# Kernel tuning notes

Hardware: AMD Instinct MI355X
Metric: run time of the kernel (lower is better)

Reference implementation:

```python
import jax, jax.numpy as jnp
import numpy as np

CLASS_NUM = 4            # number of positive classes
NUM_CLASSES = CLASS_NUM + 1  # last column is the negative class
W_P = 4.0
EPS = 1e-9
THR = 0.5


def setup_inputs() -> dict:
    key = jax.random.key(0)
    k1, k2 = jax.random.split(key)
    N = 4_000_000
    x = jax.random.normal(k1, (N, NUM_CLASSES), dtype=jnp.float32)
    t = jax.random.randint(k2, (N,), 0, NUM_CLASSES)
    return {"x": x, "t": t}


def _conf_mpu_loss(x, t):
    N = x.shape[0]
    p = jax.nn.softmax(x, axis=1)                       # [N, C]
    log_pneg = jnp.log(p[:, -1] + EPS)                  # [N]

    ones = jnp.ones((N,), dtype=jnp.float32)
    counts = jax.ops.segment_sum(ones, t, num_segments=NUM_CLASSES)  # per-class counts
    prior = counts[:CLASS_NUM] / N                      # empirical priors (positive classes)

    # loss_per_class: sum over samples with t==c of -log(p[n,c]+eps)
    logp_t = jnp.log(jnp.take_along_axis(p, t[:, None], axis=1)[:, 0] + EPS)
    class_losses = jax.ops.segment_sum(-logp_t, t, num_segments=NUM_CLASSES)

    # loss_per_class_neg: sum over samples with t==i (i positive) of -log(p_neg+eps)
    loss_neg = jax.ops.segment_sum(-log_pneg, t, num_segments=NUM_CLASSES)[:CLASS_NUM]

    # conf_loss_per_class
    conf = []
    for i in range(CLASS_NUM):
        mask = (p[:, i] > THR) & (t == i)
        nsel = jnp.sum(mask.astype(jnp.float32))
        li = jnp.sum(jnp.where(mask, -log_pneg / p[:, i], 0.0))
        conf.append(li / jnp.maximum(nsel, 1.0))        # li==0 when nsel==0
    mask_n = jnp.all(p <= THR, axis=1) & (t == CLASS_NUM)
    li_n = jnp.sum(jnp.where(mask_n, -log_pneg, 0.0))
    conf_neg = li_n / jnp.maximum(counts[CLASS_NUM], 1.0)  # li_n==0 when no selection
    conf_pos = jnp.stack(conf)                          # [CLASS_NUM]

    denom = jnp.maximum(1.0, counts[:CLASS_NUM])
    risk1 = jnp.sum(prior * class_losses[:CLASS_NUM] / denom)
    risk2 = jnp.sum(prior * conf_pos)
    risk3 = jnp.sum(prior * loss_neg / denom)
    risk4 = conf_neg

    positive_risk = W_P * (risk1 + risk2 - risk3)
    positive_risk = jnp.where(positive_risk < 0, 0.0, positive_risk)
    return positive_risk + risk4


def reference(x, t):
    return _conf_mpu_loss(x, t)
```

## Files before the change

### kernel.cpp

```cpp
#include <hip/hip_runtime.h>

namespace {
constexpr int BLOCK = 256;
constexpr float WPF = 4.0f;
constexpr float LN2 = 0.69314718055994531f;
constexpr float LOG2E = 1.44269504088896340f;
}

__device__ __forceinline__ float wave_reduce(float v) {
#pragma unroll
    for (int o = 32; o > 0; o >>= 1) v += __shfl_down(v, o, 64);
    return v;
}

__global__ __launch_bounds__(BLOCK) void mpu_main(const float* __restrict__ x,
                                                  const int* __restrict__ t,
                                                  float* __restrict__ acc, int N) {
    __shared__ float red[BLOCK / 64][16];

    float S13 = 0.f, li0 = 0.f, li1 = 0.f, li2 = 0.f, li3 = 0.f, liN = 0.f;
    int c0 = 0, c1 = 0, c2 = 0, c3 = 0, n0 = 0, n1 = 0, n2 = 0, n3 = 0;

    auto process = [&](float x0, float x1, float x2, float x3, float x4, int tc) {
        const float y0 = x0 * LOG2E, y1 = x1 * LOG2E, y2 = x2 * LOG2E,
                    y3 = x3 * LOG2E, y4 = x4 * LOG2E;
        const float f0 = __builtin_amdgcn_exp2f(y0);
        const float f1 = __builtin_amdgcn_exp2f(y1);
        const float f2 = __builtin_amdgcn_exp2f(y2);
        const float f3 = __builtin_amdgcn_exp2f(y3);
        const float f4 = __builtin_amdgcn_exp2f(y4);
        const float s = ((f0 + f1) + (f2 + f3)) + f4;
        const float L2 = __builtin_amdgcn_logf(s);
        const float thr = L2 - 1.0f;
        const float ymax = fmaxf(fmaxf(fmaxf(y0, y1), fmaxf(y2, y3)), y4);
        const float yt = (tc == 0) ? y0 : (tc == 1) ? y1 : (tc == 2) ? y2
                       : (tc == 3) ? y3 : y4;
        const float nltY = L2 - yt;
        const float nlnY = L2 - y4;
        const bool sel = (yt > thr);
        const bool alle = (ymax <= thr);
        const bool tpos = (tc < 4);
        S13 += tpos ? (y4 - yt) : 0.f;
        const float cv = sel ? nlnY * __builtin_amdgcn_exp2f(nltY) : 0.f;
        li0 += (tc == 0) ? cv : 0.f;
        li1 += (tc == 1) ? cv : 0.f;
        li2 += (tc == 2) ? cv : 0.f;
        li3 += (tc == 3) ? cv : 0.f;
        liN += (tc == 4 && alle) ? nlnY : 0.f;

        const unsigned long long b0 = __ballot(tc == 0);
        const unsigned long long b1 = __ballot(tc == 1);
        const unsigned long long b2 = __ballot(tc == 2);
        const unsigned long long b3 = __ballot(tc == 3);
        const unsigned long long bs = __ballot(sel);
        c0 += (int)__popcll(b0);
        c1 += (int)__popcll(b1);
        c2 += (int)__popcll(b2);
        c3 += (int)__popcll(b3);
        n0 += (int)__popcll(bs & b0);
        n1 += (int)__popcll(bs & b1);
        n2 += (int)__popcll(bs & b2);
        n3 += (int)__popcll(bs & b3);
    };

    const int pid = blockIdx.x * BLOCK + threadIdx.x;
    const int nQuad = N >> 2;

    if (pid < nQuad) {
        const float4* xv = reinterpret_cast<const float4*>(x) + (size_t)pid * 5;
        const float4 v0 = xv[0], v1 = xv[1], v2 = xv[2], v3 = xv[3], v4 = xv[4];
        const int4 ta = reinterpret_cast<const int4*>(t)[pid];
        process(v0.x, v0.y, v0.z, v0.w, v1.x, ta.x);
        process(v1.y, v1.z, v1.w, v2.x, v2.y, ta.y);
        process(v2.z, v2.w, v3.x, v3.y, v3.z, ta.z);
        process(v3.w, v4.x, v4.y, v4.z, v4.w, ta.w);
    }
    if (blockIdx.x == 0 && threadIdx.x == 0) {
        for (int k = (N >> 2) << 2; k < N; ++k)
            process(x[k * 5 + 0], x[k * 5 + 1], x[k * 5 + 2], x[k * 5 + 3],
                    x[k * 5 + 4], t[k]);
    }

    const int wv = threadIdx.x >> 6, ln = threadIdx.x & 63;
    float fr[6] = {S13, li0, li1, li2, li3, liN};
#pragma unroll
    for (int j = 0; j < 6; ++j) {
        const float v = wave_reduce(fr[j]);
        if (ln == 0) red[wv][j] = v;
    }
    if (ln == 0) {
        red[wv][6] = (float)c0;   red[wv][7] = (float)c1;
        red[wv][8] = (float)c2;   red[wv][9] = (float)c3;
        red[wv][10] = (float)n0;  red[wv][11] = (float)n1;
        red[wv][12] = (float)n2;  red[wv][13] = (float)n3;
    }
    __syncthreads();
    if (threadIdx.x < 14) {
        const float v = red[0][threadIdx.x] + red[1][threadIdx.x] +
                        red[2][threadIdx.x] + red[3][threadIdx.x];
        atomicAdd(&acc[threadIdx.x], v);
    }
}

__global__ void mpu_final(const float* __restrict__ acc, float* __restrict__ out, int N) {
    if (threadIdx.x == 0 && blockIdx.x == 0) {
        const float invN = 1.0f / (float)N;
        const float risk13 = LN2 * acc[0] * invN;
        float risk2 = 0.0f;
#pragma unroll
        for (int c = 0; c < 4; ++c)
            risk2 += (acc[6 + c] * invN) *
                     (LN2 * acc[1 + c] / fmaxf(acc[10 + c], 1.0f));
        const float c4 = (float)N - (acc[6] + acc[7] + acc[8] + acc[9]);
        const float risk4 = LN2 * acc[5] / fmaxf(c4, 1.0f);
        float pos = WPF * (risk13 + risk2);
        if (pos < 0.0f) pos = 0.0f;
        out[0] = pos + risk4;
    }
}

extern "C" void kernel_launch(void* const* d_in, const int* in_sizes, int n_in,
                              void* d_out, int out_size, void* d_ws, size_t ws_size,
                              hipStream_t stream) {
    const float* x = (const float*)d_in[0];
    const int* t = (const int*)d_in[1];
    float* out = (float*)d_out;
    float* acc = (float*)d_ws;
    const int N = in_sizes[1];

    hipMemsetAsync(acc, 0, 64, stream);

    const int nQuad = N >> 2;
    int grid = (nQuad + BLOCK - 1) / BLOCK;
    if (grid < 1) grid = 1;
    mpu_main<<<grid, BLOCK, 0, stream>>>(x, t, acc, N);
    mpu_final<<<1, 64, 0, stream>>>(acc, out, N);
}
```

Baseline: 159.1 us.

## Use persistent grid-stride loop with double-buffered quad prefetch

Caps the grid at 1024 blocks and has each thread walk several quads in a grid-stride loop. Loads for the next quad are issued before the current one is processed, with sched_barriers keeping that order. This cuts the number of atomics and block launches and overlaps memory latency with the exp/log math. The cost is higher register pressure from two live Quad buffers and possibly lower occupancy.

Measured after the change: 134.1 us. 15.7% less time.

```diff
diff --git a/kernel.cpp b/kernel.cpp
--- a/kernel.cpp
+++ b/kernel.cpp
@@ -2,10 +2,13 @@
 
 namespace {
 constexpr int BLOCK = 256;
+constexpr int GRID = 1024;
 constexpr float WPF = 4.0f;
 constexpr float LN2 = 0.69314718055994531f;
 constexpr float LOG2E = 1.44269504088896340f;
 }
+
+struct Quad { float4 v0, v1, v2, v3, v4; int4 tt; };
 
 __device__ __forceinline__ float wave_reduce(float v) {
 #pragma unroll
@@ -63,18 +66,38 @@
         n3 += (int)__popcll(bs & b3);
     };
 
+    auto load_quad = [&](int g, Quad& q) {
+        const float4* xv = reinterpret_cast<const float4*>(x) + (size_t)g * 5;
+        q.v0 = xv[0]; q.v1 = xv[1]; q.v2 = xv[2]; q.v3 = xv[3]; q.v4 = xv[4];
+        q.tt = reinterpret_cast<const int4*>(t)[g];
+    };
+
+    auto process4 = [&](const Quad& q) {
+        process(q.v0.x, q.v0.y, q.v0.z, q.v0.w, q.v1.x, q.tt.x);
+        process(q.v1.y, q.v1.z, q.v1.w, q.v2.x, q.v2.y, q.tt.y);
+        process(q.v2.z, q.v2.w, q.v3.x, q.v3.y, q.v3.z, q.tt.z);
+        process(q.v3.w, q.v4.x, q.v4.y, q.v4.z, q.v4.w, q.tt.w);
+    };
+
     const int pid = blockIdx.x * BLOCK + threadIdx.x;
+    const int S = gridDim.x * BLOCK;
     const int nQuad = N >> 2;
+    const int niter = (nQuad + S - 1) / S;
 
-    if (pid < nQuad) {
-        const float4* xv = reinterpret_cast<const float4*>(x) + (size_t)pid * 5;
-        const float4 v0 = xv[0], v1 = xv[1], v2 = xv[2], v3 = xv[3], v4 = xv[4];
-        const int4 ta = reinterpret_cast<const int4*>(t)[pid];
-        process(v0.x, v0.y, v0.z, v0.w, v1.x, ta.x);
-        process(v1.y, v1.z, v1.w, v2.x, v2.y, ta.y);
-        process(v2.z, v2.w, v3.x, v3.y, v3.z, ta.z);
-        process(v3.w, v4.x, v4.y, v4.z, v4.w, ta.w);
+    Quad A, B;
+    if (pid < nQuad) load_quad(pid, A);
+    for (int it = 0; it < niter; it += 2) {
+        const int g1 = pid + (it + 1) * S;
+        if (g1 < nQuad) load_quad(g1, B);
+        __builtin_amdgcn_sched_barrier(0);
+        const int gA = pid + it * S;
+        if (gA < nQuad) process4(A);
+        const int g2 = pid + (it + 2) * S;
+        if (g2 < nQuad) load_quad(g2, A);
+        __builtin_amdgcn_sched_barrier(0);
+        if (g1 < nQuad) process4(B);
     }
+
     if (blockIdx.x == 0 && threadIdx.x == 0) {
         for (int k = (N >> 2) << 2; k < N; ++k)
             process(x[k * 5 + 0], x[k * 5 + 1], x[k * 5 + 2], x[k * 5 + 3],
@@ -132,6 +155,7 @@
 
     const int nQuad = N >> 2;
     int grid = (nQuad + BLOCK - 1) / BLOCK;
+    if (grid > GRID) grid = GRID;
     if (grid < 1) grid = 1;
     mpu_main<<<grid, BLOCK, 0, stream>>>(x, t, acc, N);
     mpu_final<<<1, 64, 0, stream>>>(acc, out, N);
```
